# Optimization experiments

Measured on AMD Instinct MI355X. Metric: run time of the kernel, lower is better.

The kernel has to match this reference:

```python
import jax, jax.numpy as jnp
import numpy as np

BN_EPS = 1e-5
K = 3  # number of nearest neighbors for interpolation


def setup_inputs() -> dict:
    key = jax.random.key(0)
    ks = jax.random.split(key, 16)
    B, N1, N2 = 8, 8192, 2048
    C2, C1, H = 256, 128, 256  # in_channels, skip_channels, out_channels
    total_in = C2 + C1
    inp = {
        "xyz1": jax.random.normal(ks[0], (B, 3, N1), dtype=jnp.float32),
        "xyz2": jax.random.normal(ks[1], (B, 3, N2), dtype=jnp.float32),
        "features1": jax.random.normal(ks[2], (B, C1, N1), dtype=jnp.float32),
        "features2": jax.random.normal(ks[3], (B, C2, N2), dtype=jnp.float32),
        # SharedMLP([total_in, H, H]): two 1x1 Conv1d + BatchNorm1d (eval mode) + ReLU
        "w1": jax.random.normal(ks[4], (H, total_in), dtype=jnp.float32) * 0.05,
        "b1": jax.random.normal(ks[5], (H,), dtype=jnp.float32) * 0.01,
        "g1": 1.0 + 0.1 * jax.random.normal(ks[6], (H,), dtype=jnp.float32),
        "be1": 0.1 * jax.random.normal(ks[7], (H,), dtype=jnp.float32),
        "m1": 0.1 * jax.random.normal(ks[8], (H,), dtype=jnp.float32),
        "v1": 0.5 + jax.random.uniform(ks[9], (H,), dtype=jnp.float32),
        "w2": jax.random.normal(ks[10], (H, H), dtype=jnp.float32) * 0.05,
        "b2": jax.random.normal(ks[11], (H,), dtype=jnp.float32) * 0.01,
        "g2": 1.0 + 0.1 * jax.random.normal(ks[12], (H,), dtype=jnp.float32),
        "be2": 0.1 * jax.random.normal(ks[13], (H,), dtype=jnp.float32),
        "m2": 0.1 * jax.random.normal(ks[14], (H,), dtype=jnp.float32),
        "v2": 0.5 + jax.random.uniform(ks[15], (H,), dtype=jnp.float32),
    }
    return inp


def _conv_bn_relu(x, w, b, g, be, m, v):
    # x: [B, Cin, N], w: [Cout, Cin] (1x1 conv), BN in eval mode
    y = jnp.einsum("oc,bcn->bon", w, x) + b[None, :, None]
    y = (y - m[None, :, None]) * (g / jnp.sqrt(v + BN_EPS))[None, :, None] + be[None, :, None]
    return jax.nn.relu(y)


def reference(xyz1, xyz2, features1, features2,
              w1, b1, g1, be1, m1, v1,
              w2, b2, g2, be2, m2, v2):
    # --- squared pairwise distances [B, N1, N2] ---
    x1 = jnp.transpose(xyz1, (0, 2, 1))  # [B, N1, 3]
    x2 = jnp.transpose(xyz2, (0, 2, 1))  # [B, N2, 3]
    sq = (jnp.sum(x1 * x1, axis=-1, keepdims=True)
          + jnp.sum(x2 * x2, axis=-1)[:, None, :]
          - 2.0 * jnp.einsum("bnd,bmd->bnm", x1, x2))
    # --- k=3 nearest neighbors (smallest sq distances) ---
    neg_d, idx = jax.lax.top_k(-sq, K)          # [B, N1, K]
    dist = jnp.maximum(-neg_d, 1e-10)
    weight = 1.0 / dist
    weight = weight / jnp.sum(weight, axis=-1, keepdims=True)  # [B, N1, K]
    # --- gather neighbor features and inverse-distance interpolate ---
    feat2_t = jnp.transpose(features2, (0, 2, 1))              # [B, N2, C2]
    neighbor = jax.vmap(lambda f, i: f[i])(feat2_t, idx)       # [B, N1, K, C2]
    interp = jnp.einsum("bnkc,bnk->bnc", neighbor, weight)     # [B, N1, C2]
    interp = jnp.transpose(interp, (0, 2, 1))                  # [B, C2, N1]
    # --- concat skip features and shared MLP ---
    x = jnp.concatenate([interp, features1], axis=1)           # [B, C2+C1, N1]
    x = _conv_bn_relu(x, w1, b1, g1, be1, m1, v1)
    x = _conv_bn_relu(x, w2, b2, g2, be2, m2, v2)
    return x
```

## Files before the change

kernel.cpp:

```cpp
#include <hip/hip_runtime.h>
#include <hip/hip_bf16.h>

typedef unsigned short u16;
typedef __attribute__((ext_vector_type(4))) float f32x4;
typedef __attribute__((ext_vector_type(8))) short short8;

#define BN_EPS 1e-5f

__device__ __forceinline__ u16 f2b(float x) {
  union { float f; unsigned int u; } v; v.f = x;
  unsigned int r = (v.u + 0x7FFFu + ((v.u >> 16) & 1u)) >> 16;
  return (u16)r;
}
__device__ __forceinline__ float b2f(u16 u) {
  union { unsigned int u; float f; } v; v.u = ((unsigned int)u) << 16;
  return v.f;
}

__global__ void prep_kernel(const float* __restrict__ w1, const float* __restrict__ b1,
                            const float* __restrict__ g1, const float* __restrict__ be1,
                            const float* __restrict__ m1, const float* __restrict__ v1,
                            const float* __restrict__ w2, const float* __restrict__ b2,
                            const float* __restrict__ g2, const float* __restrict__ be2,
                            const float* __restrict__ m2, const float* __restrict__ v2,
                            u16* __restrict__ w1b, u16* __restrict__ w2b,
                            float* __restrict__ al1, float* __restrict__ bt1,
                            float* __restrict__ al2, float* __restrict__ bt2) {
  int t = threadIdx.x;
  int blk = blockIdx.x;
  if (blk < 384) {
    int id = blk * 256 + t;
    unsigned o = (unsigned)id / 384u;
    unsigned c = (unsigned)id % 384u;
    w1b[(c >> 5) * 8192 + o * 32 + (c & 31)] = f2b(w1[id]);
  } else if (blk < 640) {
    int j = (blk - 384) * 256 + t;
    unsigned o = (unsigned)j >> 8;
    unsigned c = (unsigned)j & 255u;
    w2b[(c >> 5) * 8192 + o * 32 + (c & 31)] = f2b(w2[j]);
  } else if (blk == 640) {
    float a = g1[t] / sqrtf(v1[t] + BN_EPS);
    al1[t] = a;
    bt1[t] = (b1[t] - m1[t]) * a + be1[t];
  } else {
    float a = g2[t] / sqrtf(v2[t] + BN_EPS);
    al2[t] = a;
    bt2[t] = (b2[t] - m2[t]) * a + be2[t];
  }
}

__global__ void transpose_f2_kernel(const float* __restrict__ f2, u16* __restrict__ f2t) {
  __shared__ float tile[32][33];
  int t = threadIdx.x;
  int tx = t & 31, ty = t >> 5;
  int b = blockIdx.z;
  int n2t = blockIdx.x * 32, ct = blockIdx.y * 32;
#pragma unroll
  for (int i = 0; i < 4; ++i) {
    int c = ct + ty + i * 8;
    tile[ty + i * 8][tx] = f2[((size_t)b * 256 + c) * 2048 + n2t + tx];
  }
  __syncthreads();
#pragma unroll
  for (int i = 0; i < 4; ++i) {
    int n2 = n2t + ty + i * 8;
    f2t[((size_t)b * 2048 + n2) * 256 + ct + tx] = f2b(tile[tx][ty + i * 8]);
  }
}

__global__ __launch_bounds__(256) void knn_interp_kernel(
    const float* __restrict__ xyz1, const float* __restrict__ xyz2,
    const float* __restrict__ f1, const u16* __restrict__ f2t,
    u16* __restrict__ xb) {
  union Lds {
    struct { float4 pts[2048]; float md[256 * 3]; int mi[256 * 3]; } a;
    float f1t[128 * 65];
  };
  __shared__ Lds lds;
  __shared__ float wts[64 * 3];
  __shared__ int idxs[64 * 3];

  int t = threadIdx.x;
  int b = blockIdx.x >> 7;
  int n1_0 = (blockIdx.x & 127) * 64;
  int panel = blockIdx.x;

  const float* x2 = xyz2 + b * 3 * 2048;
  for (int j = t; j < 2048; j += 256) {
    float cx = x2[j], cy = x2[2048 + j], cz = x2[4096 + j];
    float nsq = (cx * cx + cy * cy) + cz * cz;
    lds.a.pts[j] = make_float4(cx, cy, cz, nsq);
  }
  __syncthreads();

  {
    int p = t & 63, s = t >> 6;
    int n1 = n1_0 + p;
    const float* x1 = xyz1 + b * 3 * 8192;
    float bx = x1[n1], by = x1[8192 + n1], bz = x1[16384 + n1];
    float n1sq = (bx * bx + by * by) + bz * bz;
    float nx = -2.f * bx, ny = -2.f * by, nz = -2.f * bz;
    float d0 = 3.4e38f, d1 = 3.4e38f, d2 = 3.4e38f;
    int i0 = 0, i1 = 0, i2 = 0;
    int jb = s * 512;
#pragma unroll 4
    for (int jj = 0; jj < 512; ++jj) {
      float4 c = lds.a.pts[jb + jj];
      float sq = fmaf(nx, c.x, fmaf(ny, c.y, fmaf(nz, c.z, n1sq + c.w)));
      int j = jb + jj;
      bool c0 = sq < d0, c1 = sq < d1, c2 = sq < d2;
      d2 = c1 ? d1 : (c2 ? sq : d2);  i2 = c1 ? i1 : (c2 ? j : i2);
      d1 = c0 ? d0 : (c1 ? sq : d1); i1 = c0 ? i0 : (c1 ? j : i1);
      d0 = c0 ? sq : d0;             i0 = c0 ? j : i0;
    }
    lds.a.md[t * 3 + 0] = d0; lds.a.md[t * 3 + 1] = d1; lds.a.md[t * 3 + 2] = d2;
    lds.a.mi[t * 3 + 0] = i0; lds.a.mi[t * 3 + 1] = i1; lds.a.mi[t * 3 + 2] = i2;
  }
  __syncthreads();
  if (t < 64) {
    float d0 = 3.4e38f, d1 = 3.4e38f, d2 = 3.4e38f;
    int i0 = 0, i1 = 0, i2 = 0;
#pragma unroll
    for (int s = 0; s < 4; ++s) {
#pragma unroll
      for (int k = 0; k < 3; ++k) {
        float d = lds.a.md[(s * 64 + t) * 3 + k];
        int i = lds.a.mi[(s * 64 + t) * 3 + k];
        bool c0 = d < d0, c1 = d < d1, c2 = d < d2;
        i2 = c1 ? i1 : (c2 ? i : i2);
        i1 = c0 ? i0 : (c1 ? i : i1);
        i0 = c0 ? i : i0;
        d2 = c1 ? d1 : (c2 ? d : d2);
        d1 = c0 ? d0 : (c1 ? d : d1);
        d0 = c0 ? d : d0;
      }
    }
    float e0 = fmaxf(d0, 1e-10f), e1 = fmaxf(d1, 1e-10f), e2 = fmaxf(d2, 1e-10f);
    float w0 = 1.0f / e0, w1 = 1.0f / e1, w2 = 1.0f / e2;
    float sm = (w0 + w1) + w2;
    wts[t * 3 + 0] = w0 / sm; wts[t * 3 + 1] = w1 / sm; wts[t * 3 + 2] = w2 / sm;
    idxs[t * 3 + 0] = i0 * 256; idxs[t * 3 + 1] = i1 * 256; idxs[t * 3 + 2] = i2 * 256;
  }
  __syncthreads();

  {
    const u16* f2tb = f2t + (size_t)b * 2048 * 256;
    size_t xbase = (size_t)panel * 24576 + (size_t)((t >> 5) * 2048) + (t & 31);
#pragma unroll 4
    for (int p = 0; p < 64; ++p) {
      int j0 = idxs[p * 3 + 0], j1 = idxs[p * 3 + 1], j2 = idxs[p * 3 + 2];
      float w0 = wts[p * 3 + 0], w1 = wts[p * 3 + 1], w2 = wts[p * 3 + 2];
      float v = (w0 * b2f(f2tb[j0 + t]) + w1 * b2f(f2tb[j1 + t]))
                + w2 * b2f(f2tb[j2 + t]);
      xb[xbase + p * 32] = f2b(v);
    }
  }
  __syncthreads();

  {
    const float* f1b = f1 + (size_t)b * 128 * 8192 + n1_0;
    for (int it = 0; it < 32; ++it) {
      int c = it * 4 + (t >> 6);
      int n = t & 63;
      lds.f1t[c * 65 + n] = f1b[(size_t)c * 8192 + n];
    }
    __syncthreads();
    for (int it = 0; it < 32; ++it) {
      int v = it * 256 + t;
      int c = v & 127, p = v >> 7;
      float val = lds.f1t[c * 65 + p];
      xb[(size_t)panel * 24576 + (size_t)(8 + (c >> 5)) * 2048 + p * 32 + (c & 31)] = f2b(val);
    }
  }
}

__global__ __launch_bounds__(256) void gemm_fused_kernel(
    const u16* __restrict__ xin, const u16* __restrict__ w1b,
    const u16* __restrict__ w2b,
    const float* __restrict__ al1, const float* __restrict__ bt1,
    const float* __restrict__ al2, const float* __restrict__ bt2,
    float* __restrict__ fout) {
  __shared__ u16 y1t[8 * 64 * 40];
  int t = threadIdx.x;
  int panel = blockIdx.x;
  int w = t >> 6, lane = t & 63, l15 = lane & 15, quad = lane >> 4;

  f32x4 acc[4][4];
#pragma unroll
  for (int m = 0; m < 4; ++m)
#pragma unroll
    for (int n = 0; n < 4; ++n)
      acc[m][n] = (f32x4){0.f, 0.f, 0.f, 0.f};

  {
    const u16* aw = w1b + (size_t)(w * 64 + l15) * 32 + quad * 8;
    const u16* bx = xin + (size_t)panel * (12 * 2048) + (size_t)l15 * 32 + quad * 8;
    short8 af[2][4], bf[2][4];
#pragma unroll
    for (int m = 0; m < 4; ++m)
      af[0][m] = *(const short8*)(aw + m * 512);
#pragma unroll
    for (int n = 0; n < 4; ++n)
      bf[0][n] = *(const short8*)(bx + n * 512);
#pragma unroll
    for (int kt = 0; kt < 12; ++kt) {
      int cur = kt & 1, nxt = cur ^ 1;
      if (kt < 11) {
#pragma unroll
        for (int m = 0; m < 4; ++m)
          af[nxt][m] = *(const short8*)(aw + (kt + 1) * 8192 + m * 512);
#pragma unroll
        for (int n = 0; n < 4; ++n)
          bf[nxt][n] = *(const short8*)(bx + (kt + 1) * 2048 + n * 512);
      }
#pragma unroll
      for (int m = 0; m < 4; ++m)
#pragma unroll
        for (int n = 0; n < 4; ++n)
          acc[m][n] = __builtin_amdgcn_mfma_f32_16x16x32_bf16(af[cur][m], bf[cur][n], acc[m][n], 0, 0, 0);
    }
  }

  {
    float al[4][4], bt[4][4];
#pragma unroll
    for (int m = 0; m < 4; ++m)
#pragma unroll
      for (int r = 0; r < 4; ++r) {
        int o = w * 64 + m * 16 + quad * 4 + r;
        al[m][r] = al1[o];
        bt[m][r] = bt1[o];
      }
#pragma unroll
    for (int m = 0; m < 4; ++m) {
      int kt2 = w * 2 + (m >> 1);
      int osub = (m & 1) * 16 + quad * 4;
#pragma unroll
      for (int n = 0; n < 4; ++n) {
        int col = n * 16 + l15;
        ushort4 pk;
        pk.x = f2b(fmaxf(fmaf(al[m][0], acc[m][n][0], bt[m][0]), 0.f));
        pk.y = f2b(fmaxf(fmaf(al[m][1], acc[m][n][1], bt[m][1]), 0.f));
        pk.z = f2b(fmaxf(fmaf(al[m][2], acc[m][n][2], bt[m][2]), 0.f));
        pk.w = f2b(fmaxf(fmaf(al[m][3], acc[m][n][3], bt[m][3]), 0.f));
        *(ushort4*)&y1t[(kt2 * 64 + col) * 40 + osub] = pk;
      }
    }
  }
  __syncthreads();

#pragma unroll
  for (int m = 0; m < 4; ++m)
#pragma unroll
    for (int n = 0; n < 4; ++n)
      acc[m][n] = (f32x4){0.f, 0.f, 0.f, 0.f};
  {
    const u16* aw = w2b + (size_t)(w * 64 + l15) * 32 + quad * 8;
    short8 af[2][4];
#pragma unroll
    for (int m = 0; m < 4; ++m)
      af[0][m] = *(const short8*)(aw + m * 512);
#pragma unroll
    for (int kt = 0; kt < 8; ++kt) {
      int cur = kt & 1, nxt = cur ^ 1;
      if (kt < 7) {
#pragma unroll
        for (int m = 0; m < 4; ++m)
          af[nxt][m] = *(const short8*)(aw + (kt + 1) * 8192 + m * 512);
      }
      short8 bf[4];
#pragma unroll
      for (int n = 0; n < 4; ++n)
        bf[n] = *(const short8*)&y1t[(kt * 64 + n * 16 + l15) * 40 + quad * 8];
#pragma unroll
      for (int m = 0; m < 4; ++m)
#pragma unroll
        for (int n = 0; n < 4; ++n)
          acc[m][n] = __builtin_amdgcn_mfma_f32_16x16x32_bf16(af[cur][m], bf[n], acc[m][n], 0, 0, 0);
    }
  }

  {
    float al[4][4], bt[4][4];
#pragma unroll
    for (int m = 0; m < 4; ++m)
#pragma unroll
      for (int r = 0; r < 4; ++r) {
        int o = w * 64 + m * 16 + quad * 4 + r;
        al[m][r] = al2[o];
        bt[m][r] = bt2[o];
      }
    int bb = panel >> 7;
    int n1base = (panel & 127) * 64;
#pragma unroll
    for (int m = 0; m < 4; ++m)
#pragma unroll
      for (int n = 0; n < 4; ++n) {
        int col = n * 16 + l15;
#pragma unroll
        for (int r = 0; r < 4; ++r) {
          int o = w * 64 + m * 16 + quad * 4 + r;
          float vv = fmaxf(fmaf(al[m][r], acc[m][n][r], bt[m][r]), 0.f);
          fout[(size_t)(bb * 256 + o) * 8192 + n1base + col] = vv;
        }
      }
  }
}

extern "C" void kernel_launch(void* const* d_in, const int* in_sizes, int n_in,
                              void* d_out, int out_size, void* d_ws, size_t ws_size,
                              hipStream_t stream) {
  const float* xyz1 = (const float*)d_in[0];
  const float* xyz2 = (const float*)d_in[1];
  const float* f1   = (const float*)d_in[2];
  const float* f2   = (const float*)d_in[3];
  const float* w1   = (const float*)d_in[4];
  const float* b1   = (const float*)d_in[5];
  const float* g1   = (const float*)d_in[6];
  const float* be1  = (const float*)d_in[7];
  const float* m1   = (const float*)d_in[8];
  const float* v1   = (const float*)d_in[9];
  const float* w2   = (const float*)d_in[10];
  const float* b2   = (const float*)d_in[11];
  const float* g2   = (const float*)d_in[12];
  const float* be2  = (const float*)d_in[13];
  const float* m2   = (const float*)d_in[14];
  const float* v2   = (const float*)d_in[15];

  char* ws = (char*)d_ws;
  u16* xb   = (u16*)(ws);
  u16* f2t  = (u16*)(ws + 50331648);
  u16* w1b  = (u16*)(ws + 83886080);
  u16* w2b  = (u16*)(ws + 84082688);
  float* al1 = (float*)(ws + 84213760);
  float* bt1 = (float*)(ws + 84214784);
  float* al2 = (float*)(ws + 84215808);
  float* bt2 = (float*)(ws + 84216832);
  float* out = (float*)d_out;

  prep_kernel<<<642, 256, 0, stream>>>(w1, b1, g1, be1, m1, v1,
                                       w2, b2, g2, be2, m2, v2,
                                       w1b, w2b, al1, bt1, al2, bt2);
  transpose_f2_kernel<<<dim3(64, 8, 8), 256, 0, stream>>>(f2, f2t);
  knn_interp_kernel<<<1024, 256, 0, stream>>>(xyz1, xyz2, f1, f2t, xb);
  gemm_fused_kernel<<<1024, 256, 0, stream>>>(xb, w1b, w2b, al1, bt1, al2, bt2, out);
}
```

Before: 231.5 us.

## Use med3 for top-3 insertion and split GEMM panel across 8 waves

The KNN inner loop now updates the sorted distance triple with fmed3/fmin instead of nested selects, which cuts per-candidate ALU work. The fused two-layer GEMM kernel goes from 4 to 8 waves per block: each wave covers 64 output channels by 32 columns rather than 64 by 64, and the explicit double-buffered prefetch is replaced by a plain loop unrolled twice. The aim is fewer registers per wave and more waves to hide latency. In exchange each block loads the weight tiles twice and loses the manual prefetching.

```diff
diff --git a/kernel.cpp b/kernel.cpp
--- a/kernel.cpp
+++ b/kernel.cpp
@@ -109,9 +109,12 @@
       float sq = fmaf(nx, c.x, fmaf(ny, c.y, fmaf(nz, c.z, n1sq + c.w)));
       int j = jb + jj;
       bool c0 = sq < d0, c1 = sq < d1, c2 = sq < d2;
-      d2 = c1 ? d1 : (c2 ? sq : d2);  i2 = c1 ? i1 : (c2 ? j : i2);
-      d1 = c0 ? d0 : (c1 ? sq : d1); i1 = c0 ? i0 : (c1 ? j : i1);
-      d0 = c0 ? sq : d0;             i0 = c0 ? j : i0;
+      i2 = c1 ? i1 : (c2 ? j : i2);
+      i1 = c0 ? i0 : (c1 ? j : i1);
+      i0 = c0 ? j : i0;
+      d2 = __builtin_amdgcn_fmed3f(sq, d1, d2);
+      d1 = __builtin_amdgcn_fmed3f(sq, d0, d1);
+      d0 = fminf(sq, d0);
     }
     lds.a.md[t * 3 + 0] = d0; lds.a.md[t * 3 + 1] = d1; lds.a.md[t * 3 + 2] = d2;
     lds.a.mi[t * 3 + 0] = i0; lds.a.mi[t * 3 + 1] = i1; lds.a.mi[t * 3 + 2] = i2;
@@ -174,7 +177,7 @@
   }
 }
 
-__global__ __launch_bounds__(256) void gemm_fused_kernel(
+__global__ __launch_bounds__(512, 4) void gemm_fused_kernel(
     const u16* __restrict__ xin, const u16* __restrict__ w1b,
     const u16* __restrict__ w2b,
     const float* __restrict__ al1, const float* __restrict__ bt1,
@@ -184,60 +187,53 @@
   int t = threadIdx.x;
   int panel = blockIdx.x;
   int w = t >> 6, lane = t & 63, l15 = lane & 15, quad = lane >> 4;
-
-  f32x4 acc[4][4];
+  int wo = w & 3, wn = w >> 2;
+
+  f32x4 acc[4][2];
 #pragma unroll
   for (int m = 0; m < 4; ++m)
 #pragma unroll
-    for (int n = 0; n < 4; ++n)
+    for (int n = 0; n < 2; ++n)
       acc[m][n] = (f32x4){0.f, 0.f, 0.f, 0.f};
 
   {
-    const u16* aw = w1b + (size_t)(w * 64 + l15) * 32 + quad * 8;
-    const u16* bx = xin + (size_t)panel * (12 * 2048) + (size_t)l15 * 32 + quad * 8;
-    short8 af[2][4], bf[2][4];
+    const u16* aw = w1b + (size_t)(wo * 64 + l15) * 32 + quad * 8;
+    const u16* bx = xin + (size_t)panel * (12 * 2048) +
+                    (size_t)(wn * 32 + l15) * 32 + quad * 8;
+#pragma unroll 2
+    for (int kt = 0; kt < 12; ++kt) {
+      short8 af[4], bf[2];
+#pragma unroll
+      for (int m = 0; m < 4; ++m)
+        af[m] = *(const short8*)(aw + kt * 8192 + m * 512);
+#pragma unroll
+      for (int n = 0; n < 2; ++n)
+        bf[n] = *(const short8*)(bx + kt * 2048 + n * 512);
+#pragma unroll
+      for (int m = 0; m < 4; ++m)
+#pragma unroll
+        for (int n = 0; n < 2; ++n)
+          acc[m][n] = __builtin_amdgcn_mfma_f32_16x16x32_bf16(af[m], bf[n], acc[m][n], 0, 0, 0);
+    }
+  }
+
+  {
+    float al[4][4], bt[4][4];
 #pragma unroll
     for (int m = 0; m < 4; ++m)
-      af[0][m] = *(const short8*)(aw + m * 512);
-#pragma unroll
-    for (int n = 0; n < 4; ++n)
-      bf[0][n] = *(const short8*)(bx + n * 512);
-#pragma unroll
-    for (int kt = 0; kt < 12; ++kt) {
-      int cur = kt & 1, nxt = cur ^ 1;
-      if (kt < 11) {
-#pragma unroll
-        for (int m = 0; m < 4; ++m)
-          af[nxt][m] = *(const short8*)(aw + (kt + 1) * 8192 + m * 512);
-#pragma unroll
-        for (int n = 0; n < 4; ++n)
-          bf[nxt][n] = *(const short8*)(bx + (kt + 1) * 2048 + n * 512);
-      }
-#pragma unroll
-      for (int m = 0; m < 4; ++m)
-#pragma unroll
-        for (int n = 0; n < 4; ++n)
-          acc[m][n] = __builtin_amdgcn_mfma_f32_16x16x32_bf16(af[cur][m], bf[cur][n], acc[m][n], 0, 0, 0);
-    }
-  }
-
-  {
-    float al[4][4], bt[4][4];
-#pragma unroll
-    for (int m = 0; m < 4; ++m)
 #pragma unroll
       for (int r = 0; r < 4; ++r) {
-        int o = w * 64 + m * 16 + quad * 4 + r;
+        int o = wo * 64 + m * 16 + quad * 4 + r;
         al[m][r] = al1[o];
         bt[m][r] = bt1[o];
       }
 #pragma unroll
     for (int m = 0; m < 4; ++m) {
-      int kt2 = w * 2 + (m >> 1);
+      int kt2 = wo * 2 + (m >> 1);
       int osub = (m & 1) * 16 + quad * 4;
 #pragma unroll
-      for (int n = 0; n < 4; ++n) {
-        int col = n * 16 + l15;
+      for (int n = 0; n < 2; ++n) {
+        int col = wn * 32 + n * 16 + l15;
         ushort4 pk;
         pk.x = f2b(fmaxf(fmaf(al[m][0], acc[m][n][0], bt[m][0]), 0.f));
         pk.y = f2b(fmaxf(fmaf(al[m][1], acc[m][n][1], bt[m][1]), 0.f));
@@ -252,41 +248,34 @@
 #pragma unroll
   for (int m = 0; m < 4; ++m)
 #pragma unroll
-    for (int n = 0; n < 4; ++n)
+    for (int n = 0; n < 2; ++n)
       acc[m][n] = (f32x4){0.f, 0.f, 0.f, 0.f};
   {
-    const u16* aw = w2b + (size_t)(w * 64 + l15) * 32 + quad * 8;
-    short8 af[2][4];
+    const u16* aw = w2b + (size_t)(wo * 64 + l15) * 32 + quad * 8;
+#pragma unroll 2
+    for (int kt = 0; kt < 8; ++kt) {
+      short8 af[4], bf[2];
+#pragma unroll
+      for (int m = 0; m < 4; ++m)
+        af[m] = *(const short8*)(aw + kt * 8192 + m * 512);
+#pragma unroll
+      for (int n = 0; n < 2; ++n)
+        bf[n] = *(const short8*)&y1t[(kt * 64 + wn * 32 + n * 16 + l15) * 40 + quad * 8];
+#pragma unroll
+      for (int m = 0; m < 4; ++m)
+#pragma unroll
+        for (int n = 0; n < 2; ++n)
+          acc[m][n] = __builtin_amdgcn_mfma_f32_16x16x32_bf16(af[m], bf[n], acc[m][n], 0, 0, 0);
+    }
+  }
+
+  {
+    float al[4][4], bt[4][4];
 #pragma unroll
     for (int m = 0; m < 4; ++m)
-      af[0][m] = *(const short8*)(aw + m * 512);
-#pragma unroll
-    for (int kt = 0; kt < 8; ++kt) {
-      int cur = kt & 1, nxt = cur ^ 1;
-      if (kt < 7) {
-#pragma unroll
-        for (int m = 0; m < 4; ++m)
-          af[nxt][m] = *(const short8*)(aw + (kt + 1) * 8192 + m * 512);
-      }
-      short8 bf[4];
-#pragma unroll
-      for (int n = 0; n < 4; ++n)
-        bf[n] = *(const short8*)&y1t[(kt * 64 + n * 16 + l15) * 40 + quad * 8];
-#pragma unroll
-      for (int m = 0; m < 4; ++m)
-#pragma unroll
-        for (int n = 0; n < 4; ++n)
-          acc[m][n] = __builtin_amdgcn_mfma_f32_16x16x32_bf16(af[cur][m], bf[n], acc[m][n], 0, 0, 0);
-    }
-  }
-
-  {
-    float al[4][4], bt[4][4];
-#pragma unroll
-    for (int m = 0; m < 4; ++m)
 #pragma unroll
       for (int r = 0; r < 4; ++r) {
-        int o = w * 64 + m * 16 + quad * 4 + r;
+        int o = wo * 64 + m * 16 + quad * 4 + r;
         al[m][r] = al2[o];
         bt[m][r] = bt2[o];
       }
@@ -295,11 +284,11 @@
 #pragma unroll
     for (int m = 0; m < 4; ++m)
 #pragma unroll
-      for (int n = 0; n < 4; ++n) {
-        int col = n * 16 + l15;
+      for (int n = 0; n < 2; ++n) {
+        int col = wn * 32 + n * 16 + l15;
 #pragma unroll
         for (int r = 0; r < 4; ++r) {
-          int o = w * 64 + m * 16 + quad * 4 + r;
+          int o = wo * 64 + m * 16 + quad * 4 + r;
           float vv = fmaxf(fmaf(al[m][r], acc[m][n][r], bt[m][r]), 0.f);
           fout[(size_t)(bb * 256 + o) * 8192 + n1base + col] = vv;
         }
@@ -343,5 +332,5 @@
                                        w1b, w2b, al1, bt1, al2, bt2);
   transpose_f2_kernel<<<dim3(64, 8, 8), 256, 0, stream>>>(f2, f2t);
   knn_interp_kernel<<<1024, 256, 0, stream>>>(xyz1, xyz2, f1, f2t, xb);
-  gemm_fused_kernel<<<1024, 256, 0, stream>>>(xb, w1b, w2b, al1, bt1, al2, bt2, out);
-}
+  gemm_fused_kernel<<<1024, 512, 0, stream>>>(xb, w1b, w2b, al1, bt1, al2, bt2, out);
+}
```

Result: slower. 251.6 us (+8.7%).

## Fuse KNN interpolation into MLP GEMM kernel and merge prep with transpose

Applied to the files above, without the earlier changes.

Merges the weight-prep and f2 transpose kernels into one launch, and fuses the KNN interpolation kernel with the two-layer MLP GEMM kernel. The interpolated features stay in LDS and feed the first GEMM directly, so only the skip features pass through a global scratch buffer. It also swaps the top-3 distance update to fmed3/fmin and removes the explicit double-buffered register prefetch in the GEMM loops. Launch overhead and the global write and read of the interpolated activations should drop, at the cost of about 75KB of LDS per block, which lowers occupancy for the KNN phase.

```diff
diff --git a/kernel.cpp b/kernel.cpp
--- a/kernel.cpp
+++ b/kernel.cpp
@@ -17,79 +17,87 @@
   return v.f;
 }
 
-__global__ void prep_kernel(const float* __restrict__ w1, const float* __restrict__ b1,
-                            const float* __restrict__ g1, const float* __restrict__ be1,
-                            const float* __restrict__ m1, const float* __restrict__ v1,
-                            const float* __restrict__ w2, const float* __restrict__ b2,
-                            const float* __restrict__ g2, const float* __restrict__ be2,
-                            const float* __restrict__ m2, const float* __restrict__ v2,
-                            u16* __restrict__ w1b, u16* __restrict__ w2b,
-                            float* __restrict__ al1, float* __restrict__ bt1,
-                            float* __restrict__ al2, float* __restrict__ bt2) {
+__global__ void prep_transpose_kernel(
+    const float* __restrict__ f2, u16* __restrict__ f2t,
+    const float* __restrict__ w1, const float* __restrict__ b1,
+    const float* __restrict__ g1, const float* __restrict__ be1,
+    const float* __restrict__ m1, const float* __restrict__ v1,
+    const float* __restrict__ w2, const float* __restrict__ b2,
+    const float* __restrict__ g2, const float* __restrict__ be2,
+    const float* __restrict__ m2, const float* __restrict__ v2,
+    u16* __restrict__ w1b, u16* __restrict__ w2b,
+    float* __restrict__ al1, float* __restrict__ bt1,
+    float* __restrict__ al2, float* __restrict__ bt2) {
+  __shared__ float tile[32][33];
   int t = threadIdx.x;
   int blk = blockIdx.x;
-  if (blk < 384) {
-    int id = blk * 256 + t;
-    unsigned o = (unsigned)id / 384u;
-    unsigned c = (unsigned)id % 384u;
-    w1b[(c >> 5) * 8192 + o * 32 + (c & 31)] = f2b(w1[id]);
-  } else if (blk < 640) {
-    int j = (blk - 384) * 256 + t;
-    unsigned o = (unsigned)j >> 8;
-    unsigned c = (unsigned)j & 255u;
-    w2b[(c >> 5) * 8192 + o * 32 + (c & 31)] = f2b(w2[j]);
-  } else if (blk == 640) {
-    float a = g1[t] / sqrtf(v1[t] + BN_EPS);
-    al1[t] = a;
-    bt1[t] = (b1[t] - m1[t]) * a + be1[t];
+  if (blk < 4096) {
+    int b = blk >> 9, rem = blk & 511;
+    int n2t = (rem & 63) * 32, ct = (rem >> 6) * 32;
+    int tx = t & 31, ty = t >> 5;
+#pragma unroll
+    for (int i = 0; i < 4; ++i) {
+      int c = ct + ty + i * 8;
+      tile[ty + i * 8][tx] = f2[((size_t)b * 256 + c) * 2048 + n2t + tx];
+    }
+    __syncthreads();
+#pragma unroll
+    for (int i = 0; i < 4; ++i) {
+      int n2 = n2t + ty + i * 8;
+      f2t[((size_t)b * 2048 + n2) * 256 + ct + tx] = f2b(tile[tx][ty + i * 8]);
+    }
   } else {
-    float a = g2[t] / sqrtf(v2[t] + BN_EPS);
-    al2[t] = a;
-    bt2[t] = (b2[t] - m2[t]) * a + be2[t];
-  }
-}
-
-__global__ void transpose_f2_kernel(const float* __restrict__ f2, u16* __restrict__ f2t) {
-  __shared__ float tile[32][33];
-  int t = threadIdx.x;
-  int tx = t & 31, ty = t >> 5;
-  int b = blockIdx.z;
-  int n2t = blockIdx.x * 32, ct = blockIdx.y * 32;
-#pragma unroll
-  for (int i = 0; i < 4; ++i) {
-    int c = ct + ty + i * 8;
-    tile[ty + i * 8][tx] = f2[((size_t)b * 256 + c) * 2048 + n2t + tx];
-  }
-  __syncthreads();
-#pragma unroll
-  for (int i = 0; i < 4; ++i) {
-    int n2 = n2t + ty + i * 8;
-    f2t[((size_t)b * 2048 + n2) * 256 + ct + tx] = f2b(tile[tx][ty + i * 8]);
-  }
-}
-
-__global__ __launch_bounds__(256) void knn_interp_kernel(
+    int bb = blk - 4096;
+    if (bb < 384) {
+      int id = bb * 256 + t;
+      unsigned o = (unsigned)id / 384u;
+      unsigned c = (unsigned)id % 384u;
+      w1b[(c >> 5) * 8192 + o * 32 + (c & 31)] = f2b(w1[id]);
+    } else if (bb < 640) {
+      int j = (bb - 384) * 256 + t;
+      unsigned o = (unsigned)j >> 8;
+      unsigned c = (unsigned)j & 255u;
+      w2b[(c >> 5) * 8192 + o * 32 + (c & 31)] = f2b(w2[j]);
+    } else if (bb == 640) {
+      float a = g1[t] / sqrtf(v1[t] + BN_EPS);
+      al1[t] = a;
+      bt1[t] = (b1[t] - m1[t]) * a + be1[t];
+    } else {
+      float a = g2[t] / sqrtf(v2[t] + BN_EPS);
+      al2[t] = a;
+      bt2[t] = (b2[t] - m2[t]) * a + be2[t];
+    }
+  }
+}
+
+__global__ __launch_bounds__(256) void knn_gemm_kernel(
     const float* __restrict__ xyz1, const float* __restrict__ xyz2,
     const float* __restrict__ f1, const u16* __restrict__ f2t,
-    u16* __restrict__ xb) {
-  union Lds {
-    struct { float4 pts[2048]; float md[256 * 3]; int mi[256 * 3]; } a;
-    float f1t[128 * 65];
-  };
-  __shared__ Lds lds;
-  __shared__ float wts[64 * 3];
-  __shared__ int idxs[64 * 3];
+    u16* __restrict__ xbs,
+    const u16* __restrict__ w1b, const u16* __restrict__ w2b,
+    const float* __restrict__ al1, const float* __restrict__ bt1,
+    const float* __restrict__ al2, const float* __restrict__ bt2,
+    float* __restrict__ fout) {
+  __shared__ __align__(16) char raw[75264];
+  float4* pts = (float4*)raw;
+  float*  md  = (float*)(raw + 32768);
+  int*    mi  = (int*)(raw + 35840);
+  float*  f1t = (float*)raw;
+  u16*    y1t = (u16*)raw;
+  u16*    xbt = (u16*)(raw + 40960);
+  float*  wts = (float*)(raw + 73728);
+  int*    idxs = (int*)(raw + 74496);
 
   int t = threadIdx.x;
-  int b = blockIdx.x >> 7;
-  int n1_0 = (blockIdx.x & 127) * 64;
   int panel = blockIdx.x;
+  int b = panel >> 7;
+  int n1_0 = (panel & 127) * 64;
 
   const float* x2 = xyz2 + b * 3 * 2048;
   for (int j = t; j < 2048; j += 256) {
     float cx = x2[j], cy = x2[2048 + j], cz = x2[4096 + j];
     float nsq = (cx * cx + cy * cy) + cz * cz;
-    lds.a.pts[j] = make_float4(cx, cy, cz, nsq);
+    pts[j] = make_float4(cx, cy, cz, nsq);
   }
   __syncthreads();
 
@@ -105,16 +113,19 @@
     int jb = s * 512;
 #pragma unroll 4
     for (int jj = 0; jj < 512; ++jj) {
-      float4 c = lds.a.pts[jb + jj];
+      float4 c = pts[jb + jj];
       float sq = fmaf(nx, c.x, fmaf(ny, c.y, fmaf(nz, c.z, n1sq + c.w)));
       int j = jb + jj;
       bool c0 = sq < d0, c1 = sq < d1, c2 = sq < d2;
-      d2 = c1 ? d1 : (c2 ? sq : d2);  i2 = c1 ? i1 : (c2 ? j : i2);
-      d1 = c0 ? d0 : (c1 ? sq : d1); i1 = c0 ? i0 : (c1 ? j : i1);
-      d0 = c0 ? sq : d0;             i0 = c0 ? j : i0;
-    }
-    lds.a.md[t * 3 + 0] = d0; lds.a.md[t * 3 + 1] = d1; lds.a.md[t * 3 + 2] = d2;
-    lds.a.mi[t * 3 + 0] = i0; lds.a.mi[t * 3 + 1] = i1; lds.a.mi[t * 3 + 2] = i2;
+      i2 = c1 ? i1 : (c2 ? j : i2);
+      i1 = c0 ? i0 : (c1 ? j : i1);
+      i0 = c0 ? j : i0;
+      d2 = __builtin_amdgcn_fmed3f(sq, d1, d2);
+      d1 = __builtin_amdgcn_fmed3f(sq, d0, d1);
+      d0 = fminf(sq, d0);
+    }
+    md[t * 3 + 0] = d0; md[t * 3 + 1] = d1; md[t * 3 + 2] = d2;
+    mi[t * 3 + 0] = i0; mi[t * 3 + 1] = i1; mi[t * 3 + 2] = i2;
   }
   __syncthreads();
   if (t < 64) {
@@ -124,8 +135,8 @@
     for (int s = 0; s < 4; ++s) {
 #pragma unroll
       for (int k = 0; k < 3; ++k) {
-        float d = lds.a.md[(s * 64 + t) * 3 + k];
-        int i = lds.a.mi[(s * 64 + t) * 3 + k];
+        float d = md[(s * 64 + t) * 3 + k];
+        int i = mi[(s * 64 + t) * 3 + k];
         bool c0 = d < d0, c1 = d < d1, c2 = d < d2;
         i2 = c1 ? i1 : (c2 ? i : i2);
         i1 = c0 ? i0 : (c1 ? i : i1);
@@ -145,44 +156,34 @@
 
   {
     const u16* f2tb = f2t + (size_t)b * 2048 * 256;
-    size_t xbase = (size_t)panel * 24576 + (size_t)((t >> 5) * 2048) + (t & 31);
+    int xbase = (t >> 5) * 2048 + (t & 31);
 #pragma unroll 4
     for (int p = 0; p < 64; ++p) {
       int j0 = idxs[p * 3 + 0], j1 = idxs[p * 3 + 1], j2 = idxs[p * 3 + 2];
       float w0 = wts[p * 3 + 0], w1 = wts[p * 3 + 1], w2 = wts[p * 3 + 2];
       float v = (w0 * b2f(f2tb[j0 + t]) + w1 * b2f(f2tb[j1 + t]))
                 + w2 * b2f(f2tb[j2 + t]);
-      xb[xbase + p * 32] = f2b(v);
-    }
-  }
-  __syncthreads();
+      xbt[xbase + p * 32] = f2b(v);
+    }
+  }
 
   {
     const float* f1b = f1 + (size_t)b * 128 * 8192 + n1_0;
     for (int it = 0; it < 32; ++it) {
       int c = it * 4 + (t >> 6);
       int n = t & 63;
-      lds.f1t[c * 65 + n] = f1b[(size_t)c * 8192 + n];
+      f1t[c * 65 + n] = f1b[(size_t)c * 8192 + n];
     }
     __syncthreads();
+    u16* xso = xbs + (size_t)panel * 8192;
     for (int it = 0; it < 32; ++it) {
       int v = it * 256 + t;
       int c = v & 127, p = v >> 7;
-      float val = lds.f1t[c * 65 + p];
-      xb[(size_t)panel * 24576 + (size_t)(8 + (c >> 5)) * 2048 + p * 32 + (c & 31)] = f2b(val);
-    }
-  }
-}
-
-__global__ __launch_bounds__(256) void gemm_fused_kernel(
-    const u16* __restrict__ xin, const u16* __restrict__ w1b,
-    const u16* __restrict__ w2b,
-    const float* __restrict__ al1, const float* __restrict__ bt1,
-    const float* __restrict__ al2, const float* __restrict__ bt2,
-    float* __restrict__ fout) {
-  __shared__ u16 y1t[8 * 64 * 40];
-  int t = threadIdx.x;
-  int panel = blockIdx.x;
+      xso[(c >> 5) * 2048 + p * 32 + (c & 31)] = f2b(f1t[c * 65 + p]);
+    }
+  }
+  __syncthreads();
+
   int w = t >> 6, lane = t & 63, l15 = lane & 15, quad = lane >> 4;
 
   f32x4 acc[4][4];
@@ -194,30 +195,36 @@
 
   {
     const u16* aw = w1b + (size_t)(w * 64 + l15) * 32 + quad * 8;
-    const u16* bx = xin + (size_t)panel * (12 * 2048) + (size_t)l15 * 32 + quad * 8;
-    short8 af[2][4], bf[2][4];
-#pragma unroll
-    for (int m = 0; m < 4; ++m)
-      af[0][m] = *(const short8*)(aw + m * 512);
-#pragma unroll
-    for (int n = 0; n < 4; ++n)
-      bf[0][n] = *(const short8*)(bx + n * 512);
-#pragma unroll
-    for (int kt = 0; kt < 12; ++kt) {
-      int cur = kt & 1, nxt = cur ^ 1;
-      if (kt < 11) {
-#pragma unroll
-        for (int m = 0; m < 4; ++m)
-          af[nxt][m] = *(const short8*)(aw + (kt + 1) * 8192 + m * 512);
+    const u16* bxs = xbs + (size_t)panel * 8192 + (size_t)l15 * 32 + quad * 8;
+#pragma unroll 2
+    for (int kt = 0; kt < 8; ++kt) {
+      short8 af[4], bf[4];
+#pragma unroll
+      for (int m = 0; m < 4; ++m)
+        af[m] = *(const short8*)(aw + kt * 8192 + m * 512);
+#pragma unroll
+      for (int n = 0; n < 4; ++n)
+        bf[n] = *(const short8*)&xbt[kt * 2048 + (n * 16 + l15) * 32 + quad * 8];
+#pragma unroll
+      for (int m = 0; m < 4; ++m)
 #pragma unroll
         for (int n = 0; n < 4; ++n)
-          bf[nxt][n] = *(const short8*)(bx + (kt + 1) * 2048 + n * 512);
-      }
+          acc[m][n] = __builtin_amdgcn_mfma_f32_16x16x32_bf16(af[m], bf[n], acc[m][n], 0, 0, 0);
+    }
+#pragma unroll 2
+    for (int kt = 0; kt < 4; ++kt) {
+      short8 af[4], bf[4];
+#pragma unroll
+      for (int m = 0; m < 4; ++m)
+        af[m] = *(const short8*)(aw + (8 + kt) * 8192 + m * 512);
+#pragma unroll
+      for (int n = 0; n < 4; ++n)
+        bf[n] = *(const short8*)(bxs + kt * 2048 + n * 512);
 #pragma unroll
       for (int m = 0; m < 4; ++m)
 #pragma unroll
         for (int n = 0; n < 4; ++n)
-          acc[m][n] = __builtin_amdgcn_mfma_f32_16x16x32_bf16(af[cur][m], bf[cur][n], acc[m][n], 0, 0, 0);
+          acc[m][n] = __builtin_amdgcn_mfma_f32_16x16x32_bf16(af[m], bf[n], acc[m][n], 0, 0, 0);
     }
   }
 
@@ -256,19 +263,12 @@
       acc[m][n] = (f32x4){0.f, 0.f, 0.f, 0.f};
   {
     const u16* aw = w2b + (size_t)(w * 64 + l15) * 32 + quad * 8;
-    short8 af[2][4];
-#pragma unroll
-    for (int m = 0; m < 4; ++m)
-      af[0][m] = *(const short8*)(aw + m * 512);
-#pragma unroll
+#pragma unroll 2
     for (int kt = 0; kt < 8; ++kt) {
-      int cur = kt & 1, nxt = cur ^ 1;
-      if (kt < 7) {
-#pragma unroll
-        for (int m = 0; m < 4; ++m)
-          af[nxt][m] = *(const short8*)(aw + (kt + 1) * 8192 + m * 512);
-      }
-      short8 bf[4];
+      short8 af[4], bf[4];
+#pragma unroll
+      for (int m = 0; m < 4; ++m)
+        af[m] = *(const short8*)(aw + kt * 8192 + m * 512);
 #pragma unroll
       for (int n = 0; n < 4; ++n)
         bf[n] = *(const short8*)&y1t[(kt * 64 + n * 16 + l15) * 40 + quad * 8];
@@ -276,7 +276,7 @@
       for (int m = 0; m < 4; ++m)
 #pragma unroll
         for (int n = 0; n < 4; ++n)
-          acc[m][n] = __builtin_amdgcn_mfma_f32_16x16x32_bf16(af[cur][m], bf[n], acc[m][n], 0, 0, 0);
+          acc[m][n] = __builtin_amdgcn_mfma_f32_16x16x32_bf16(af[m], bf[n], acc[m][n], 0, 0, 0);
     }
   }
 
@@ -328,8 +328,8 @@
   const float* v2   = (const float*)d_in[15];
 
   char* ws = (char*)d_ws;
-  u16* xb   = (u16*)(ws);
-  u16* f2t  = (u16*)(ws + 50331648);
+  u16* xbs  = (u16*)(ws);
+  u16* f2t  = (u16*)(ws + 16777216);
   u16* w1b  = (u16*)(ws + 83886080);
   u16* w2b  = (u16*)(ws + 84082688);
   float* al1 = (float*)(ws + 84213760);
@@ -338,10 +338,9 @@
   float* bt2 = (float*)(ws + 84216832);
   float* out = (float*)d_out;
 
-  prep_kernel<<<642, 256, 0, stream>>>(w1, b1, g1, be1, m1, v1,
-                                       w2, b2, g2, be2, m2, v2,
-                                       w1b, w2b, al1, bt1, al2, bt2);
-  transpose_f2_kernel<<<dim3(64, 8, 8), 256, 0, stream>>>(f2, f2t);
-  knn_interp_kernel<<<1024, 256, 0, stream>>>(xyz1, xyz2, f1, f2t, xb);
-  gemm_fused_kernel<<<1024, 256, 0, stream>>>(xb, w1b, w2b, al1, bt1, al2, bt2, out);
-}
+  prep_transpose_kernel<<<4738, 256, 0, stream>>>(
+      f2, f2t, w1, b1, g1, be1, m1, v1, w2, b2, g2, be2, m2, v2,
+      w1b, w2b, al1, bt1, al2, bt2);
+  knn_gemm_kernel<<<1024, 256, 0, stream>>>(
+      xyz1, xyz2, f1, f2t, xbs, w1b, w2b, al1, bt1, al2, bt2, out);
+}
```

Result: slower. 240.3 us (+3.8%).
